# Kernel optimization log

Measured on AMD Instinct MI355X. Metric: run time of the kernel, lower is better.

## Reference

```python
import jax, jax.numpy as jnp
import numpy as np

N, E = 50000, 600000
IN, H, OUT = 128, 256, 64
BN_EPS = 1e-5
NEG_SLOPE = 0.01  # F.leaky_relu default


def _gin_conv(x, eps, W1, b1, W2, b2, src, dst):
    # sum aggregation over incoming edges, then 2-layer MLP
    agg = jax.ops.segment_sum(x[src], dst, num_segments=N)  # [N, d]
    h = (1.0 + eps) * x + agg
    h = jax.nn.relu(h @ W1 + b1) @ W2 + b2
    return h


def setup_inputs() -> dict:
    key = jax.random.key(0)
    ks = jax.random.split(key, 16)

    def w(k, shape):
        return (jax.random.normal(k, shape, jnp.float32) / np.sqrt(shape[0])).astype(jnp.float32)

    x = jax.random.normal(ks[0], (N, IN), jnp.float32)
    src = jax.random.randint(ks[1], (E,), 0, N, dtype=jnp.int64)
    dst = jax.random.randint(ks[2], (E,), 0, N, dtype=jnp.int64)
    edge_index = jnp.stack([src, dst])

    return {
        "x": x,
        "edge_index": edge_index,
        # conv0: Linear(IN,H), ReLU, Linear(H,H); trainable eps
        "eps0": jnp.float32(0.0),
        "W01": w(ks[3], (IN, H)), "b01": jnp.zeros((H,), jnp.float32),
        "W02": w(ks[4], (H, H)), "b02": jnp.zeros((H,), jnp.float32),
        # conv1 (middle): eps fixed at 0 (train_eps=False)
        "W11": w(ks[5], (H, H)), "b11": jnp.zeros((H,), jnp.float32),
        "W12": w(ks[6], (H, H)), "b12": jnp.zeros((H,), jnp.float32),
        # conv2 (last): Linear(H,H), ReLU, Linear(H,OUT); trainable eps
        "eps2": jnp.float32(0.0),
        "W21": w(ks[7], (H, H)), "b21": jnp.zeros((H,), jnp.float32),
        "W22": w(ks[8], (H, OUT)), "b22": jnp.zeros((OUT,), jnp.float32),
        # shared BatchNorm1d(H) buffers/params (eval mode)
        "bn_gamma": jnp.ones((H,), jnp.float32),
        "bn_beta": jnp.zeros((H,), jnp.float32),
        "bn_mean": jnp.zeros((H,), jnp.float32),
        "bn_var": jnp.ones((H,), jnp.float32),
    }


def reference(x, edge_index, eps0, W01, b01, W02, b02,
              W11, b11, W12, b12, eps2, W21, b21, W22, b22,
              bn_gamma, bn_beta, bn_mean, bn_var):
    src, dst = edge_index[0], edge_index[1]

    def bn_lrelu(h):
        h = (h - bn_mean) * jax.lax.rsqrt(bn_var + BN_EPS) * bn_gamma + bn_beta
        return jnp.where(h >= 0, h, NEG_SLOPE * h)  # dropout is identity in eval

    h = _gin_conv(x, eps0, W01, b01, W02, b02, src, dst)
    h = bn_lrelu(h)
    h = _gin_conv(h, jnp.float32(0.0), W11, b11, W12, b12, src, dst)
    h = bn_lrelu(h)
    h = _gin_conv(h, eps2, W21, b21, W22, b22, src, dst)
    return h  # [N, OUT]
```

## Files before the change

kernel.cpp:

```cpp
#include <hip/hip_runtime.h>

typedef unsigned short u16;
typedef unsigned int u32;
typedef __attribute__((ext_vector_type(8))) unsigned short u16x8;

constexpr int IN_F = 128;
constexpr int HID  = 256;
constexpr int OUT_F = 64;

static inline int cdiv_i(long long a, long long b) { return (int)((a + b - 1) / b); }

__device__ inline float b2f(u16 h) { return __uint_as_float(((u32)h) << 16); }
__device__ inline u16 f2b(float f) {
    u32 u = __float_as_uint(f);
    u32 r = (u + 0x7FFFu + ((u >> 16) & 1u)) >> 16;
    return (u16)r;
}

__global__ __launch_bounds__(256) void deg_count_kernel(
    const int* __restrict__ ei, int* __restrict__ deg, int E)
{
    int e = blockIdx.x * blockDim.x + threadIdx.x;
    if (e >= E) return;
    atomicAdd(&deg[ei[E + e]], 1);
}

__global__ __launch_bounds__(1024) void block_scan_kernel(
    const int* __restrict__ deg, int* __restrict__ row_ptr,
    int* __restrict__ blksum, int Nn)
{
    __shared__ int buf[1024];
    int i = blockIdx.x * 1024 + threadIdx.x;
    int v = (i < Nn) ? deg[i] : 0;
    buf[threadIdx.x] = v;
    __syncthreads();
    for (int off = 1; off < 1024; off <<= 1) {
        int t = (threadIdx.x >= off) ? buf[threadIdx.x - off] : 0;
        __syncthreads();
        buf[threadIdx.x] += t;
        __syncthreads();
    }
    if (i < Nn) row_ptr[i] = buf[threadIdx.x] - v;
    if (threadIdx.x == 1023) blksum[blockIdx.x] = buf[1023];
}

__global__ __launch_bounds__(1024) void scan_blksums_kernel(
    int* __restrict__ blksum, int nblk)
{
    __shared__ int buf[1024];
    int v = (threadIdx.x < nblk) ? blksum[threadIdx.x] : 0;
    buf[threadIdx.x] = v;
    __syncthreads();
    for (int off = 1; off < 1024; off <<= 1) {
        int t = (threadIdx.x >= off) ? buf[threadIdx.x - off] : 0;
        __syncthreads();
        buf[threadIdx.x] += t;
        __syncthreads();
    }
    if (threadIdx.x < nblk) blksum[threadIdx.x] = buf[threadIdx.x] - v;
}

__global__ __launch_bounds__(1024) void add_offsets_kernel(
    int* __restrict__ row_ptr, int* __restrict__ cursor,
    const int* __restrict__ blksum, int Nn, int E)
{
    int i = blockIdx.x * 1024 + threadIdx.x;
    if (i < Nn) {
        int r = row_ptr[i] + blksum[i >> 10];
        row_ptr[i] = r;
        cursor[i]  = r;
    } else if (i == Nn) {
        row_ptr[Nn] = E;
    }
}

__global__ __launch_bounds__(256) void csr_fill_kernel(
    const int* __restrict__ ei, int* __restrict__ cursor,
    int* __restrict__ csr_src, int E)
{
    int e = blockIdx.x * blockDim.x + threadIdx.x;
    if (e >= E) return;
    int d = ei[E + e];
    int pos = atomicAdd(&cursor[d], 1);
    csr_src[pos] = ei[e];
}

__global__ __launch_bounds__(256) void xconv_kernel(
    const float4* __restrict__ in, ushort4* __restrict__ out, long long total4)
{
    long long i = (long long)blockIdx.x * blockDim.x + threadIdx.x;
    if (i >= total4) return;
    float4 v = in[i];
    ushort4 o;
    o.x = f2b(v.x); o.y = f2b(v.y); o.z = f2b(v.z); o.w = f2b(v.w);
    out[i] = o;
}

__global__ __launch_bounds__(256) void wconv_all_kernel(
    const float* __restrict__ W01, const float* __restrict__ W02,
    const float* __restrict__ W11, const float* __restrict__ W12,
    const float* __restrict__ W21, const float* __restrict__ W22,
    u16* __restrict__ Wt01, u16* __restrict__ Wt02,
    u16* __restrict__ Wt11, u16* __restrict__ Wt12,
    u16* __restrict__ Wt21, u16* __restrict__ Wt22)
{
    int id = blockIdx.x * blockDim.x + threadIdx.x;
    const float* W; u16* Wt; int kshift, NC;
    if (id < 32768)                  { W = W01; Wt = Wt01; kshift = 7; NC = 256; }
    else if ((id -= 32768) < 65536)  { W = W02; Wt = Wt02; kshift = 8; NC = 256; }
    else if ((id -= 65536) < 65536)  { W = W11; Wt = Wt11; kshift = 8; NC = 256; }
    else if ((id -= 65536) < 65536)  { W = W12; Wt = Wt12; kshift = 8; NC = 256; }
    else if ((id -= 65536) < 65536)  { W = W21; Wt = Wt21; kshift = 8; NC = 256; }
    else if ((id -= 65536) < 16384)  { W = W22; Wt = Wt22; kshift = 8; NC = 64;  }
    else return;
    int K = 1 << kshift;
    int n = id >> kshift;
    int k = id & (K - 1);
    Wt[id] = f2b(W[(long long)k * NC + n]);
}

__global__ __launch_bounds__(256) void agg256_bf16(
    const u16x8* __restrict__ x, const int* __restrict__ row_ptr,
    const int* __restrict__ csr_src, const float* __restrict__ eps_ptr,
    u16x8* __restrict__ out, int Nn)
{
    int n = blockIdx.x * 4 + (threadIdx.x >> 6);
    if (n >= Nn) return;
    int lane = threadIdx.x & 63;
    int grp = lane >> 5;
    int sl  = lane & 31;
    size_t off = (size_t)n * 32 + sl;
    float acc[8];
    if (grp == 0) {
        float e1 = 1.0f + (eps_ptr ? *eps_ptr : 0.0f);
        u16x8 xv = x[off];
#pragma unroll
        for (int i = 0; i < 8; ++i) acc[i] = e1 * b2f(xv[i]);
    } else {
#pragma unroll
        for (int i = 0; i < 8; ++i) acc[i] = 0.0f;
    }
    int end = row_ptr[n + 1];
    int j = row_ptr[n] + grp;
    for (; j + 2 < end; j += 4) {
        int s0 = csr_src[j], s1 = csr_src[j + 2];
        u16x8 v0 = x[(size_t)s0 * 32 + sl];
        u16x8 v1 = x[(size_t)s1 * 32 + sl];
#pragma unroll
        for (int i = 0; i < 8; ++i) acc[i] += b2f(v0[i]) + b2f(v1[i]);
    }
    if (j < end) {
        u16x8 v = x[(size_t)csr_src[j] * 32 + sl];
#pragma unroll
        for (int i = 0; i < 8; ++i) acc[i] += b2f(v[i]);
    }
#pragma unroll
    for (int i = 0; i < 8; ++i) acc[i] += __shfl_xor(acc[i], 32, 64);
    if (grp == 0) {
        u16x8 o;
#pragma unroll
        for (int i = 0; i < 8; ++i) o[i] = f2b(acc[i]);
        out[off] = o;
    }
}

__global__ __launch_bounds__(256) void agg128_bf16(
    const u16x8* __restrict__ x, const int* __restrict__ row_ptr,
    const int* __restrict__ csr_src, const float* __restrict__ eps_ptr,
    u16x8* __restrict__ out, int Nn)
{
    int n = blockIdx.x * 4 + (threadIdx.x >> 6);
    if (n >= Nn) return;
    int lane = threadIdx.x & 63;
    int grp = lane >> 4;
    int sl  = lane & 15;
    size_t off = (size_t)n * 16 + sl;
    float acc[8];
    if (grp == 0) {
        float e1 = 1.0f + (eps_ptr ? *eps_ptr : 0.0f);
        u16x8 xv = x[off];
#pragma unroll
        for (int i = 0; i < 8; ++i) acc[i] = e1 * b2f(xv[i]);
    } else {
#pragma unroll
        for (int i = 0; i < 8; ++i) acc[i] = 0.0f;
    }
    int end = row_ptr[n + 1];
    int j = row_ptr[n] + grp;
    for (; j + 4 < end; j += 8) {
        int s0 = csr_src[j], s1 = csr_src[j + 4];
        u16x8 v0 = x[(size_t)s0 * 16 + sl];
        u16x8 v1 = x[(size_t)s1 * 16 + sl];
#pragma unroll
        for (int i = 0; i < 8; ++i) acc[i] += b2f(v0[i]) + b2f(v1[i]);
    }
    if (j < end) {
        u16x8 v = x[(size_t)csr_src[j] * 16 + sl];
#pragma unroll
        for (int i = 0; i < 8; ++i) acc[i] += b2f(v[i]);
    }
#pragma unroll
    for (int i = 0; i < 8; ++i) {
        acc[i] += __shfl_xor(acc[i], 16, 64);
        acc[i] += __shfl_xor(acc[i], 32, 64);
    }
    if (grp == 0) {
        u16x8 o;
#pragma unroll
        for (int i = 0; i < 8; ++i) o[i] = f2b(acc[i]);
        out[off] = o;
    }
}

using bf16x8 = __attribute__((ext_vector_type(8))) short;
using f32x4  = __attribute__((ext_vector_type(4))) float;

__device__ inline void gload_lds16(const void* g, void* l) {
    __builtin_amdgcn_global_load_lds(
        (const __attribute__((address_space(1))) u32*)g,
        (__attribute__((address_space(3))) u32*)l, 16, 0, 0);
}

template <int K, int BM, int BN, int WM, int WN, int FUSE, bool OUT_F32>
__global__ __launch_bounds__(WM* WN * 64) void gemm_mfma(
    const u16* __restrict__ A, const u16* __restrict__ Wt,
    const float* __restrict__ bias,
    const float* __restrict__ bn_g, const float* __restrict__ bn_b,
    const float* __restrict__ bn_m, const float* __restrict__ bn_v,
    void* __restrict__ Cout, int M, int NC)
{
    __shared__ u16 As[BM * 64];
    __shared__ u16 Bs[BN * 64];

    constexpr int NW = WM * WN;
    const int tid = threadIdx.x;
    const int wave = tid >> 6;
    const int lane = tid & 63;
    const int wm = wave / WN;
    const int wn = wave % WN;
    const int m0 = blockIdx.x * BM;
    const int n0 = blockIdx.y * BN;
    const int l15 = lane & 15;
    const int l4  = lane >> 4;

    f32x4 acc[4][4] = {};

    for (int k0 = 0; k0 < K; k0 += 64) {
        constexpr int AIW = (BM / 8) / NW;
#pragma unroll
        for (int i = 0; i < AIW; ++i) {
            int inst = wave * AIW + i;
            int g = inst * 64 + lane;
            int row = g >> 3;
            int cb = (g & 7) ^ (row & 7);
            int grow = m0 + row;
            if (grow >= M) grow = M - 1;
            gload_lds16(A + (size_t)grow * K + k0 + cb * 8, As + inst * 512);
        }
        constexpr int BIW = (BN / 8) / NW;
#pragma unroll
        for (int i = 0; i < BIW; ++i) {
            int inst = wave * BIW + i;
            int g = inst * 64 + lane;
            int row = g >> 3;
            int cb = (g & 7) ^ (row & 7);
            gload_lds16(Wt + (size_t)(n0 + row) * K + k0 + cb * 8, Bs + inst * 512);
        }
        __syncthreads();

#pragma unroll
        for (int kk = 0; kk < 2; ++kk) {
            bf16x8 af[4], bf[4];
#pragma unroll
            for (int m = 0; m < 4; ++m) {
                int row = wm * 64 + m * 16 + l15;
                int cb = kk * 4 + l4;
                af[m] = *(const bf16x8*)(As + row * 64 + ((cb ^ (row & 7)) * 8));
            }
#pragma unroll
            for (int n = 0; n < 4; ++n) {
                int row = wn * 64 + n * 16 + l15;
                int cb = kk * 4 + l4;
                bf[n] = *(const bf16x8*)(Bs + row * 64 + ((cb ^ (row & 7)) * 8));
            }
#pragma unroll
            for (int m = 0; m < 4; ++m)
#pragma unroll
                for (int n = 0; n < 4; ++n)
                    acc[m][n] = __builtin_amdgcn_mfma_f32_16x16x32_bf16(
                        af[m], bf[n], acc[m][n], 0, 0, 0);
        }
        __syncthreads();
    }

#pragma unroll
    for (int n = 0; n < 4; ++n) {
        int col = n0 + wn * 64 + n * 16 + l15;
        float bv = bias[col];
        float sc = 1.0f, sh = 0.0f;
        if (FUSE == 1) {
            float g = bn_g[col], be = bn_b[col], mm = bn_m[col], vv = bn_v[col];
            sc = g * rsqrtf(vv + 1e-5f);
            sh = be - mm * sc;
        }
#pragma unroll
        for (int m = 0; m < 4; ++m) {
            int rb = m0 + wm * 64 + m * 16 + l4 * 4;
#pragma unroll
            for (int j = 0; j < 4; ++j) {
                int gm = rb + j;
                if (gm >= M) continue;
                float v = acc[m][n][j] + bv;
                if (FUSE == 0) v = fmaxf(v, 0.0f);
                else if (FUSE == 1) {
                    v = fmaf(v, sc, sh);
                    v = v >= 0.0f ? v : 0.01f * v;
                }
                if (OUT_F32) ((float*)Cout)[(size_t)gm * NC + col] = v;
                else         ((u16*)Cout)[(size_t)gm * NC + col] = f2b(v);
            }
        }
    }
}

extern "C" void kernel_launch(void* const* d_in, const int* in_sizes, int n_in,
                              void* d_out, int out_size, void* d_ws, size_t ws_size,
                              hipStream_t stream)
{
    const float* x    = (const float*)d_in[0];
    const int*   ei   = (const int*)d_in[1];
    const float* eps0 = (const float*)d_in[2];
    const float* W01  = (const float*)d_in[3];
    const float* b01  = (const float*)d_in[4];
    const float* W02  = (const float*)d_in[5];
    const float* b02  = (const float*)d_in[6];
    const float* W11  = (const float*)d_in[7];
    const float* b11  = (const float*)d_in[8];
    const float* W12  = (const float*)d_in[9];
    const float* b12  = (const float*)d_in[10];
    const float* eps2 = (const float*)d_in[11];
    const float* W21  = (const float*)d_in[12];
    const float* b21  = (const float*)d_in[13];
    const float* W22  = (const float*)d_in[14];
    const float* b22  = (const float*)d_in[15];
    const float* bn_g = (const float*)d_in[16];
    const float* bn_b = (const float*)d_in[17];
    const float* bn_m = (const float*)d_in[18];
    const float* bn_v = (const float*)d_in[19];

    const int Nn = in_sizes[0] / IN_F;
    const int E  = in_sizes[1] / 2;

    u16* P = (u16*)d_ws;
    u16* Q = P + (size_t)Nn * HID;
    u16* Xb = Q + (size_t)Nn * HID;
    u16* Wt01 = Xb + (size_t)Nn * IN_F;
    u16* Wt02 = Wt01 + HID * IN_F;
    u16* Wt11 = Wt02 + HID * HID;
    u16* Wt12 = Wt11 + HID * HID;
    u16* Wt21 = Wt12 + HID * HID;
    u16* Wt22 = Wt21 + HID * HID;
    int* row_ptr = (int*)(Wt22 + OUT_F * HID);
    int* cursor  = row_ptr + (Nn + 1);
    int* deg     = cursor + Nn;
    int* blksum  = deg + Nn;
    int* csr_src = blksum + 1024;

    dim3 blk(256);
    const int nwave_blocks = cdiv_i(Nn, 4);
    const int nscan = cdiv_i(Nn, 1024);

    hipMemsetAsync(deg, 0, (size_t)Nn * sizeof(int), stream);
    deg_count_kernel<<<cdiv_i(E, 256), blk, 0, stream>>>(ei, deg, E);
    block_scan_kernel<<<nscan, 1024, 0, stream>>>(deg, row_ptr, blksum, Nn);
    scan_blksums_kernel<<<1, 1024, 0, stream>>>(blksum, nscan);
    add_offsets_kernel<<<cdiv_i(Nn + 1, 1024), 1024, 0, stream>>>(
        row_ptr, cursor, blksum, Nn, E);
    csr_fill_kernel<<<cdiv_i(E, 256), blk, 0, stream>>>(ei, cursor, csr_src, E);

    xconv_kernel<<<cdiv_i((long long)Nn * IN_F / 4, 256), blk, 0, stream>>>(
        (const float4*)x, (ushort4*)Xb, (long long)Nn * IN_F / 4);
    wconv_all_kernel<<<cdiv_i(32768 + 4 * 65536 + 16384, 256), blk, 0, stream>>>(
        W01, W02, W11, W12, W21, W22, Wt01, Wt02, Wt11, Wt12, Wt21, Wt22);

    const dim3 gA(cdiv_i(Nn, 128), 1);
    const dim3 gF(cdiv_i(Nn, 256), 1);
    const dim3 blk512(512);

    agg128_bf16<<<nwave_blocks, blk, 0, stream>>>(
        (const u16x8*)Xb, row_ptr, csr_src, eps0, (u16x8*)P, Nn);
    gemm_mfma<128, 128, 256, 2, 4, 0, false><<<gA, blk512, 0, stream>>>(
        P, Wt01, b01, nullptr, nullptr, nullptr, nullptr, Q, Nn, HID);
    gemm_mfma<256, 128, 256, 2, 4, 1, false><<<gA, blk512, 0, stream>>>(
        Q, Wt02, b02, bn_g, bn_b, bn_m, bn_v, P, Nn, HID);

    agg256_bf16<<<nwave_blocks, blk, 0, stream>>>(
        (const u16x8*)P, row_ptr, csr_src, nullptr, (u16x8*)Q, Nn);
    gemm_mfma<256, 128, 256, 2, 4, 0, false><<<gA, blk512, 0, stream>>>(
        Q, Wt11, b11, nullptr, nullptr, nullptr, nullptr, P, Nn, HID);
    gemm_mfma<256, 128, 256, 2, 4, 1, false><<<gA, blk512, 0, stream>>>(
        P, Wt12, b12, bn_g, bn_b, bn_m, bn_v, Q, Nn, HID);

    agg256_bf16<<<nwave_blocks, blk, 0, stream>>>(
        (const u16x8*)Q, row_ptr, csr_src, eps2, (u16x8*)P, Nn);
    gemm_mfma<256, 128, 256, 2, 4, 0, false><<<gA, blk512, 0, stream>>>(
        P, Wt21, b21, nullptr, nullptr, nullptr, nullptr, Q, Nn, HID);
    gemm_mfma<256, 256, 64, 4, 1, 2, true><<<gF, blk, 0, stream>>>(
        Q, Wt22, b22, nullptr, nullptr, nullptr, nullptr, d_out, Nn, OUT_F);
}
```

Baseline: 344.0 us.

## Fuse each GIN layer's two-GEMM MLP into one kernel with LDS-resident hidden tile

Replaces the pair of per-layer GEMM launches with a single mlp_fused kernel. Each 64-row block computes the first linear layer, applies ReLU, and keeps the bf16 hidden tile in LDS. It then multiplies that tile by the second weight matrix and applies the bias/BN/leaky-ReLU epilogue. Weight tiles are double-buffered through global_load_lds so the next K-slice loads during the current MFMA work. This removes the global write and re-read of the 256-wide hidden activation and one launch per layer. The cost is a large LDS footprint (~112KB), which limits blocks per CU, and the whole weight matrix is re-streamed for every 64-row block.

```diff
diff --git a/kernel.cpp b/kernel.cpp
--- a/kernel.cpp
+++ b/kernel.cpp
@@ -16,6 +16,7 @@
     u32 r = (u + 0x7FFFu + ((u >> 16) & 1u)) >> 16;
     return (u16)r;
 }
+__device__ inline float4 ld4(const float* p) { return *reinterpret_cast<const float4*>(p); }
 
 __global__ __launch_bounds__(256) void deg_count_kernel(
     const int* __restrict__ ei, int* __restrict__ deg, int E)
@@ -221,103 +222,183 @@
         (__attribute__((address_space(3))) u32*)l, 16, 0, 0);
 }
 
-template <int K, int BM, int BN, int WM, int WN, int FUSE, bool OUT_F32>
-__global__ __launch_bounds__(WM* WN * 64) void gemm_mfma(
-    const u16* __restrict__ A, const u16* __restrict__ Wt,
-    const float* __restrict__ bias,
+template <int KIN, int NOUT, int FUSE2, bool OF32>
+__global__ __launch_bounds__(512) void mlp_fused(
+    const u16* __restrict__ A, const u16* __restrict__ W1t,
+    const float* __restrict__ b1,
+    const u16* __restrict__ W2t, const float* __restrict__ b2,
     const float* __restrict__ bn_g, const float* __restrict__ bn_b,
     const float* __restrict__ bn_m, const float* __restrict__ bn_v,
-    void* __restrict__ Cout, int M, int NC)
-{
-    __shared__ u16 As[BM * 64];
-    __shared__ u16 Bs[BN * 64];
-
-    constexpr int NW = WM * WN;
-    const int tid = threadIdx.x;
-    const int wave = tid >> 6;
+    void* __restrict__ Cout, int M)
+{
+    __shared__ u16 lds[57344];
+    u16* Ab = lds;
+    u16* Wb = lds + 8192;
+    u16* Hl = lds + 8192 + 32768;
+
+    const int tid  = threadIdx.x;
+    const int wv   = tid >> 6;
     const int lane = tid & 63;
-    const int wm = wave / WN;
-    const int wn = wave % WN;
-    const int m0 = blockIdx.x * BM;
-    const int n0 = blockIdx.y * BN;
-    const int l15 = lane & 15;
-    const int l4  = lane >> 4;
-
-    f32x4 acc[4][4] = {};
-
-    for (int k0 = 0; k0 < K; k0 += 64) {
-        constexpr int AIW = (BM / 8) / NW;
-#pragma unroll
-        for (int i = 0; i < AIW; ++i) {
-            int inst = wave * AIW + i;
+    const int l15  = lane & 15, l4 = lane >> 4;
+    const int m0   = blockIdx.x * 64;
+
+    constexpr int KT1 = KIN / 64;
+
+    auto stageA = [&](int kt, int buf) {
+        int inst = wv;
+        int g = inst * 64 + lane;
+        int row = g >> 3;
+        int cb = (g & 7) ^ (row & 7);
+        int grow = m0 + row; if (grow >= M) grow = M - 1;
+        gload_lds16(A + (size_t)grow * KIN + kt * 64 + cb * 8,
+                    Ab + buf * 4096 + inst * 512);
+    };
+    auto stageW1 = [&](int kt, int buf) {
+#pragma unroll
+        for (int i = 0; i < 4; ++i) {
+            int inst = wv * 4 + i;
             int g = inst * 64 + lane;
             int row = g >> 3;
             int cb = (g & 7) ^ (row & 7);
-            int grow = m0 + row;
-            if (grow >= M) grow = M - 1;
-            gload_lds16(A + (size_t)grow * K + k0 + cb * 8, As + inst * 512);
-        }
-        constexpr int BIW = (BN / 8) / NW;
-#pragma unroll
-        for (int i = 0; i < BIW; ++i) {
-            int inst = wave * BIW + i;
+            gload_lds16(W1t + (size_t)row * KIN + kt * 64 + cb * 8,
+                        Wb + buf * 16384 + inst * 512);
+        }
+    };
+    auto stageW2 = [&](int kt, int buf) {
+        constexpr int I = NOUT / 64;
+#pragma unroll
+        for (int i = 0; i < I; ++i) {
+            int inst = wv * I + i;
             int g = inst * 64 + lane;
             int row = g >> 3;
             int cb = (g & 7) ^ (row & 7);
-            gload_lds16(Wt + (size_t)(n0 + row) * K + k0 + cb * 8, Bs + inst * 512);
-        }
-        __syncthreads();
-
+            gload_lds16(W2t + (size_t)row * 256 + kt * 64 + cb * 8,
+                        Wb + buf * 16384 + inst * 512);
+        }
+    };
+
+    f32x4 acc1[4][2] = {};
+    int cur = 0;
+    stageA(0, 0); stageW1(0, 0);
+    __syncthreads();
+#pragma unroll
+    for (int kt = 0; kt < KT1; ++kt) {
+        if (kt + 1 < KT1) { stageA(kt + 1, cur ^ 1); stageW1(kt + 1, cur ^ 1); }
+        else              { stageW2(0, cur ^ 1); }
 #pragma unroll
         for (int kk = 0; kk < 2; ++kk) {
-            bf16x8 af[4], bf[4];
+            int cb = kk * 4 + l4;
+            bf16x8 af[4], wf[2];
 #pragma unroll
             for (int m = 0; m < 4; ++m) {
-                int row = wm * 64 + m * 16 + l15;
-                int cb = kk * 4 + l4;
-                af[m] = *(const bf16x8*)(As + row * 64 + ((cb ^ (row & 7)) * 8));
-            }
-#pragma unroll
-            for (int n = 0; n < 4; ++n) {
-                int row = wn * 64 + n * 16 + l15;
-                int cb = kk * 4 + l4;
-                bf[n] = *(const bf16x8*)(Bs + row * 64 + ((cb ^ (row & 7)) * 8));
+                int row = m * 16 + l15;
+                af[m] = *(const bf16x8*)(Ab + cur * 4096 + row * 64 + ((cb ^ (row & 7)) * 8));
+            }
+#pragma unroll
+            for (int n = 0; n < 2; ++n) {
+                int wrow = wv * 32 + n * 16 + l15;
+                wf[n] = *(const bf16x8*)(Wb + cur * 16384 + wrow * 64 + ((cb ^ (wrow & 7)) * 8));
             }
 #pragma unroll
             for (int m = 0; m < 4; ++m)
 #pragma unroll
-                for (int n = 0; n < 4; ++n)
-                    acc[m][n] = __builtin_amdgcn_mfma_f32_16x16x32_bf16(
-                        af[m], bf[n], acc[m][n], 0, 0, 0);
-        }
-        __syncthreads();
-    }
-
-#pragma unroll
-    for (int n = 0; n < 4; ++n) {
-        int col = n0 + wn * 64 + n * 16 + l15;
-        float bv = bias[col];
-        float sc = 1.0f, sh = 0.0f;
-        if (FUSE == 1) {
-            float g = bn_g[col], be = bn_b[col], mm = bn_m[col], vv = bn_v[col];
-            sc = g * rsqrtf(vv + 1e-5f);
-            sh = be - mm * sc;
-        }
-#pragma unroll
-        for (int m = 0; m < 4; ++m) {
-            int rb = m0 + wm * 64 + m * 16 + l4 * 4;
-#pragma unroll
-            for (int j = 0; j < 4; ++j) {
-                int gm = rb + j;
-                if (gm >= M) continue;
-                float v = acc[m][n][j] + bv;
-                if (FUSE == 0) v = fmaxf(v, 0.0f);
-                else if (FUSE == 1) {
-                    v = fmaf(v, sc, sh);
-                    v = v >= 0.0f ? v : 0.01f * v;
-                }
-                if (OUT_F32) ((float*)Cout)[(size_t)gm * NC + col] = v;
-                else         ((u16*)Cout)[(size_t)gm * NC + col] = f2b(v);
+                for (int n = 0; n < 2; ++n)
+                    acc1[m][n] = __builtin_amdgcn_mfma_f32_16x16x32_bf16(
+                        wf[n], af[m], acc1[m][n], 0, 0, 0);
+        }
+        if (kt + 1 < KT1) { __syncthreads(); cur ^= 1; }
+    }
+#pragma unroll
+    for (int m = 0; m < 4; ++m) {
+        int arow = m * 16 + l15;
+#pragma unroll
+        for (int n = 0; n < 2; ++n) {
+            int hcol = wv * 32 + n * 16 + l4 * 4;
+            float4 bv = ld4(b1 + hcol);
+            float v0 = fmaxf(acc1[m][n][0] + bv.x, 0.f);
+            float v1 = fmaxf(acc1[m][n][1] + bv.y, 0.f);
+            float v2 = fmaxf(acc1[m][n][2] + bv.z, 0.f);
+            float v3 = fmaxf(acc1[m][n][3] + bv.w, 0.f);
+            u32 p0 = (u32)f2b(v0) | ((u32)f2b(v1) << 16);
+            u32 p1 = (u32)f2b(v2) | ((u32)f2b(v3) << 16);
+            int g = hcol >> 3;
+            u16* dst = Hl + arow * 256 + ((g ^ (arow & 7)) * 8) + (hcol & 7);
+            *reinterpret_cast<uint2*>(dst) = make_uint2(p0, p1);
+        }
+    }
+    __syncthreads();
+    cur ^= 1;
+
+    constexpr int MF2 = (NOUT == 256) ? 4 : 2;
+    constexpr int NF2 = (NOUT == 256) ? 2 : 1;
+    const int rbase = (NOUT == 256) ? 0 : (wv >> 2) * 32;
+    const int cbase = (NOUT == 256) ? wv * 32 : (wv & 3) * 16;
+
+    f32x4 acc2[MF2][NF2] = {};
+#pragma unroll
+    for (int kt = 0; kt < 4; ++kt) {
+        if (kt + 1 < 4) stageW2(kt + 1, cur ^ 1);
+#pragma unroll
+        for (int kk = 0; kk < 2; ++kk) {
+            int cbg = kt * 8 + kk * 4 + l4;
+            int cbw = kk * 4 + l4;
+            bf16x8 hf[MF2], wf[NF2];
+#pragma unroll
+            for (int m = 0; m < MF2; ++m) {
+                int row = rbase + m * 16 + l15;
+                hf[m] = *(const bf16x8*)(Hl + row * 256 + ((cbg ^ (row & 7)) * 8));
+            }
+#pragma unroll
+            for (int n = 0; n < NF2; ++n) {
+                int wrow = cbase + n * 16 + l15;
+                wf[n] = *(const bf16x8*)(Wb + cur * 16384 + wrow * 64 + ((cbw ^ (wrow & 7)) * 8));
+            }
+#pragma unroll
+            for (int m = 0; m < MF2; ++m)
+#pragma unroll
+                for (int n = 0; n < NF2; ++n)
+                    acc2[m][n] = __builtin_amdgcn_mfma_f32_16x16x32_bf16(
+                        wf[n], hf[m], acc2[m][n], 0, 0, 0);
+        }
+        if (kt + 1 < 4) { __syncthreads(); cur ^= 1; }
+    }
+
+#pragma unroll
+    for (int m = 0; m < MF2; ++m) {
+        int grow = m0 + rbase + m * 16 + l15;
+        if (grow >= M) continue;
+#pragma unroll
+        for (int n = 0; n < NF2; ++n) {
+            int col = cbase + n * 16 + l4 * 4;
+            float4 bv = ld4(b2 + col);
+            float v0 = acc2[m][n][0] + bv.x;
+            float v1 = acc2[m][n][1] + bv.y;
+            float v2 = acc2[m][n][2] + bv.z;
+            float v3 = acc2[m][n][3] + bv.w;
+            if (FUSE2 == 1) {
+                float4 g = ld4(bn_g + col), be = ld4(bn_b + col);
+                float4 mm = ld4(bn_m + col), vv = ld4(bn_v + col);
+                float s0 = g.x * rsqrtf(vv.x + 1e-5f);
+                float s1 = g.y * rsqrtf(vv.y + 1e-5f);
+                float s2 = g.z * rsqrtf(vv.z + 1e-5f);
+                float s3 = g.w * rsqrtf(vv.w + 1e-5f);
+                v0 = fmaf(v0, s0, be.x - mm.x * s0);
+                v1 = fmaf(v1, s1, be.y - mm.y * s1);
+                v2 = fmaf(v2, s2, be.z - mm.z * s2);
+                v3 = fmaf(v3, s3, be.w - mm.w * s3);
+                v0 = v0 >= 0.f ? v0 : 0.01f * v0;
+                v1 = v1 >= 0.f ? v1 : 0.01f * v1;
+                v2 = v2 >= 0.f ? v2 : 0.01f * v2;
+                v3 = v3 >= 0.f ? v3 : 0.01f * v3;
+            }
+            if (OF32) {
+                float4 o = make_float4(v0, v1, v2, v3);
+                *reinterpret_cast<float4*>((float*)Cout + (size_t)grow * NOUT + col) = o;
+            } else {
+                u32 p0 = (u32)f2b(v0) | ((u32)f2b(v1) << 16);
+                u32 p1 = (u32)f2b(v2) | ((u32)f2b(v3) << 16);
+                *reinterpret_cast<uint2*>((u16*)Cout + (size_t)grow * NOUT + col) =
+                    make_uint2(p0, p1);
             }
         }
     }
@@ -383,28 +464,21 @@
     wconv_all_kernel<<<cdiv_i(32768 + 4 * 65536 + 16384, 256), blk, 0, stream>>>(
         W01, W02, W11, W12, W21, W22, Wt01, Wt02, Wt11, Wt12, Wt21, Wt22);
 
-    const dim3 gA(cdiv_i(Nn, 128), 1);
-    const dim3 gF(cdiv_i(Nn, 256), 1);
+    const int mlp_blocks = cdiv_i(Nn, 64);
     const dim3 blk512(512);
 
     agg128_bf16<<<nwave_blocks, blk, 0, stream>>>(
         (const u16x8*)Xb, row_ptr, csr_src, eps0, (u16x8*)P, Nn);
-    gemm_mfma<128, 128, 256, 2, 4, 0, false><<<gA, blk512, 0, stream>>>(
-        P, Wt01, b01, nullptr, nullptr, nullptr, nullptr, Q, Nn, HID);
-    gemm_mfma<256, 128, 256, 2, 4, 1, false><<<gA, blk512, 0, stream>>>(
-        Q, Wt02, b02, bn_g, bn_b, bn_m, bn_v, P, Nn, HID);
+    mlp_fused<128, 256, 1, false><<<mlp_blocks, blk512, 0, stream>>>(
+        P, Wt01, b01, Wt02, b02, bn_g, bn_b, bn_m, bn_v, Q, Nn);
 
     agg256_bf16<<<nwave_blocks, blk, 0, stream>>>(
-        (const u16x8*)P, row_ptr, csr_src, nullptr, (u16x8*)Q, Nn);
-    gemm_mfma<256, 128, 256, 2, 4, 0, false><<<gA, blk512, 0, stream>>>(
-        Q, Wt11, b11, nullptr, nullptr, nullptr, nullptr, P, Nn, HID);
-    gemm_mfma<256, 128, 256, 2, 4, 1, false><<<gA, blk512, 0, stream>>>(
-        P, Wt12, b12, bn_g, bn_b, bn_m, bn_v, Q, Nn, HID);
+        (const u16x8*)Q, row_ptr, csr_src, nullptr, (u16x8*)P, Nn);
+    mlp_fused<256, 256, 1, false><<<mlp_blocks, blk512, 0, stream>>>(
+        P, Wt11, b11, Wt12, b12, bn_g, bn_b, bn_m, bn_v, Q, Nn);
 
     agg256_bf16<<<nwave_blocks, blk, 0, stream>>>(
         (const u16x8*)Q, row_ptr, csr_src, eps2, (u16x8*)P, Nn);
-    gemm_mfma<256, 128, 256, 2, 4, 0, false><<<gA, blk512, 0, stream>>>(
-        P, Wt21, b21, nullptr, nullptr, nullptr, nullptr, Q, Nn, HID);
-    gemm_mfma<256, 256, 64, 4, 1, 2, true><<<gF, blk, 0, stream>>>(
-        Q, Wt22, b22, nullptr, nullptr, nullptr, nullptr, d_out, Nn, OUT_F);
-}
+    mlp_fused<256, 64, 2, true><<<mlp_blocks, blk512, 0, stream>>>(
+        P, Wt21, b21, Wt22, b22, nullptr, nullptr, nullptr, nullptr, d_out, Nn);
+}
```

Measured after the change: 313.2 us. 1.1x faster.
